# Performance work log

Measured on AMD Instinct MI355X. Metric: run time of the kernel, lower is better.

## Reference

```python
import math
import jax, jax.numpy as jnp
import numpy as np

IN_CH = 64
RANK = 32
W_FREQ = 64


def setup_inputs() -> dict:
    key = jax.random.key(0)
    k1, k2, k3 = jax.random.split(key, 3)
    B, C, H, W = 8, IN_CH, 256, 512
    x = jax.random.normal(k1, (B, C, H, W), dtype=jnp.float32)
    dt = jax.random.uniform(k2, (B,), dtype=jnp.float32)
    # 1x1 conv: weight [out=2*RANK, in=C], bias [2*RANK]; init U(-0.01, 0.01) as in module
    w = jax.random.uniform(k3, (2 * RANK, C), dtype=jnp.float32, minval=-0.01, maxval=0.01)
    b = jnp.zeros((2 * RANK,), dtype=jnp.float32)
    return {"x": x, "dt": dt, "w": w, "b": b}


def reference(x, dt, w, b):
    B, C, H, W = x.shape
    # AdaptiveAvgPool2d((None, W_FREQ)): W divisible by W_FREQ -> exact block mean
    x_pool = x.reshape(B, C, H, W_FREQ, W // W_FREQ).mean(-1)  # [B,C,H,Wf]
    params = jnp.einsum('bchw,oc->bohw', x_pool, w) + b[None, :, None, None]
    nu = jax.nn.softplus(params[:, :RANK])                    # [B,R,H,Wf]
    theta = jnp.tanh(params[:, RANK:]) * math.pi              # [B,R,H,Wf]
    dtb = dt[:, None, None, None]
    decay = jnp.exp(-nu * dtb)
    angle = theta * dtb
    filt_r = (decay * jnp.cos(angle)).sum(axis=1)             # [B,H,Wf]
    filt_i = (decay * jnp.sin(angle)).sum(axis=1)
    filt = (filt_r + 1j * filt_i)[:, None, :, :]              # [B,1,H,Wf] complex64
    x_spec = jnp.fft.rfft2(x, norm='ortho')                   # [B,C,H,W//2+1]
    out_spec = jnp.concatenate([x_spec[..., :W_FREQ] * filt, x_spec[..., W_FREQ:]], axis=-1)
    return jnp.fft.irfft2(out_spec, s=(H, W), norm='ortho').astype(x.dtype)
```

## Files before the change

kernel.cpp:

```cpp
#include <hip/hip_runtime.h>
#include <cstddef>
#include <cstdint>

#define PI_F    3.14159265358979323846f
#define TWOPI_F 6.28318530717958647692f

#define ZH_OFF 16777216u
#define G_OFF  33554432u
#define TW_OFF 33816576u

typedef __attribute__((ext_vector_type(8))) short bf16x8;
typedef __attribute__((ext_vector_type(4))) float f32x4;

__device__ __forceinline__ void bsplit(float x, short& h, short& l) {
    uint32_t u  = __float_as_uint(x);
    uint32_t hb = (u + 0x7fffu + ((u >> 16) & 1u)) & 0xffff0000u;
    h = (short)(hb >> 16);
    float r = x - __uint_as_float(hb);
    uint32_t u2 = __float_as_uint(r);
    l = (short)((u2 + 0x7fffu + ((u2 >> 16) & 1u)) >> 16);
}

__global__ __launch_bounds__(256) void k_filt(const float* __restrict__ x,
                                              const float* __restrict__ dt,
                                              const float* __restrict__ wmat,
                                              const float* __restrict__ bvec,
                                              float* __restrict__ G) {
    __shared__ float pooled[64 * 65];
    __shared__ float wsh[64 * 65];
    int t = threadIdx.x;
    int b = blockIdx.x >> 8, h = blockIdx.x & 255;
    for (int i = t; i < 4096; i += 256)
        wsh[(i >> 6) * 65 + (i & 63)] = wmat[i];
    for (int c = 0; c < 64; c++) {
        const float* xr = x + (((size_t)(b * 64 + c)) * 256 + h) * 512;
        float2 v = ((const float2*)xr)[t];
        float s = v.x + v.y;
        s += __shfl_xor(s, 1);
        s += __shfl_xor(s, 2);
        if ((t & 3) == 0) pooled[c * 65 + (t >> 2)] = s * 0.125f;
    }
    __syncthreads();
    float dtb = dt[b];
    int o = t & 63, q = t >> 6;
    float bo = bvec[o];
    for (int jj = 0; jj < 16; jj++) {
        int j = q * 16 + jj;
        float acc = bo;
        #pragma unroll 16
        for (int c = 0; c < 64; c++)
            acc = fmaf(wsh[o * 65 + c], pooled[c * 65 + j], acc);
        float nl;
        if (o < 32) nl = (acc > 20.0f) ? acc : log1pf(expf(acc));
        else        nl = tanhf(acc) * PI_F;
        float other = __shfl_xor(nl, 32);
        float nu = (o < 32) ? nl : other;
        float th = (o < 32) ? other : nl;
        float decay = expf(-nu * dtb);
        float sa, ca; sincosf(th * dtb, &sa, &ca);
        float tr = decay * ca, ti = decay * sa;
        #pragma unroll
        for (int off = 1; off < 64; off <<= 1) {
            tr += __shfl_xor(tr, off);
            ti += __shfl_xor(ti, off);
        }
        if ((t & 63) == 0) {
            float2 g = make_float2(0.5f * tr - 1.0f, 0.5f * ti);
            ((float2*)G)[((size_t)b * 256 + h) * 64 + j] = g;
        }
    }
}

__global__ __launch_bounds__(256) void k_gemmA(const float* __restrict__ x,
                                               float* __restrict__ Zw) {
    __shared__ __align__(16) float As[32][68];
    __shared__ __align__(16) float Bs[32][64];
    int t = threadIdx.x;
    int row0 = blockIdx.x * 64, n0 = blockIdx.y * 64;
    int lr = t >> 3, lk4 = (t & 7) << 2;
    int bkr = t >> 4, bc4 = (t & 15) << 2;
    int ty = t >> 4, tx = t & 15;
    int wf0 = (n0 + bc4) >> 1;
    float u_r[2], u_i[2], c16r[2], c16i[2], advr[2], advi[2];
    #pragma unroll
    for (int q = 0; q < 2; q++) {
        int wf = wf0 + q;
        float s, c;
        sincosf((float)((bkr * wf) & 511) * (TWOPI_F / 512.0f), &s, &c);
        u_r[q] = c; u_i[q] = -s;
        sincosf((float)((16 * wf) & 511) * (TWOPI_F / 512.0f), &s, &c);
        c16r[q] = c; c16i[q] = -s;
        sincosf((float)((32 * wf) & 511) * (TWOPI_F / 512.0f), &s, &c);
        advr[q] = c; advi[q] = -s;
    }
    float acc[4][4] = {};
    size_t xrow0 = (size_t)(row0 + lr) * 512;
    size_t xrow1 = (size_t)(row0 + lr + 32) * 512;
    for (int k0 = 0; k0 < 512; k0 += 32) {
        __syncthreads();
        {
            float4 v = *(const float4*)(x + xrow0 + k0 + lk4);
            As[lk4 + 0][lr] = v.x; As[lk4 + 1][lr] = v.y;
            As[lk4 + 2][lr] = v.z; As[lk4 + 3][lr] = v.w;
        }
        {
            float4 v = *(const float4*)(x + xrow1 + k0 + lk4);
            int m = lr + 32;
            As[lk4 + 0][m] = v.x; As[lk4 + 1][m] = v.y;
            As[lk4 + 2][m] = v.z; As[lk4 + 3][m] = v.w;
        }
        *(float4*)&Bs[bkr][bc4] = make_float4(u_r[0], u_i[0], u_r[1], u_i[1]);
        {
            float r0 = u_r[0] * c16r[0] - u_i[0] * c16i[0];
            float i0 = u_r[0] * c16i[0] + u_i[0] * c16r[0];
            float r1 = u_r[1] * c16r[1] - u_i[1] * c16i[1];
            float i1 = u_r[1] * c16i[1] + u_i[1] * c16r[1];
            *(float4*)&Bs[bkr + 16][bc4] = make_float4(r0, i0, r1, i1);
        }
        #pragma unroll
        for (int q = 0; q < 2; q++) {
            float nr = u_r[q] * advr[q] - u_i[q] * advi[q];
            float ni = u_r[q] * advi[q] + u_i[q] * advr[q];
            u_r[q] = nr; u_i[q] = ni;
        }
        __syncthreads();
        #pragma unroll
        for (int kk = 0; kk < 32; kk++) {
            float4 ra = *(const float4*)&As[kk][ty << 2];
            float4 rb = *(const float4*)&Bs[kk][tx << 2];
            float a[4] = {ra.x, ra.y, ra.z, ra.w};
            float bq[4] = {rb.x, rb.y, rb.z, rb.w};
            #pragma unroll
            for (int i = 0; i < 4; i++)
                #pragma unroll
                for (int j = 0; j < 4; j++)
                    acc[i][j] = fmaf(a[i], bq[j], acc[i][j]);
        }
    }
    #pragma unroll
    for (int i = 0; i < 4; i++) {
        int r = row0 + (ty << 2) + i;
        *(float4*)(Zw + (size_t)r * 128 + n0 + (tx << 2)) =
            make_float4(acc[i][0], acc[i][1], acc[i][2], acc[i][3]);
    }
}

__global__ __launch_bounds__(256) void k_twid(float* __restrict__ outbase) {
    int t = blockIdx.x * 256 + threadIdx.x;
    int m = t >> 8, k = t & 255;
    float s, c;
    sincosf((float)((m * k) & 255) * (TWOPI_F / 256.0f), &s, &c);
    short ch, cl, nsh, nsl, psh, psl;
    bsplit(c, ch, cl);
    bsplit(-s, nsh, nsl);
    bsplit(s, psh, psl);
    short* fw = (short*)(outbase + TW_OFF);
    short* iv = fw + 262144;
    fw[t] = ch; fw[65536 + t] = cl; fw[131072 + t] = nsh; fw[196608 + t] = nsl;
    iv[t] = ch; iv[65536 + t] = cl; iv[131072 + t] = psh; iv[196608 + t] = psl;
}

__global__ __launch_bounds__(256) void k_cgemm_mfma(const float* __restrict__ Zin,
                                                    float* __restrict__ Zout,
                                                    const float* __restrict__ G,
                                                    const short* __restrict__ tab) {
    __shared__ short As[4][64][40];
    __shared__ short Bs[4][64][40];
    int t = threadIdx.x;
    int p  = blockIdx.x;
    int m0 = blockIdx.y * 64;
    size_t zbase = (size_t)p * 32768;
    int w = t >> 6, l = t & 63;
    int wm = w >> 1, wj = w & 1;
    int lr = l & 15, lh = l >> 4;
    int att = w;
    int bk  = t >> 3;
    int bju = t & 7;

    f32x4 accRp[2][2] = {}, accRm[2][2] = {}, accI[2][2] = {};

    #pragma unroll 1
    for (int k0 = 0; k0 < 256; k0 += 32) {
        __syncthreads();
        {
            const short* tb = tab + att * 65536 + k0;
            #pragma unroll
            for (int i = 0; i < 4; i++) {
                int c = l + 64 * i;
                int row = c >> 2, ko = (c & 3) << 3;
                int4 v = *(const int4*)(tb + (m0 + row) * 256 + ko);
                *(int4*)&As[att][row][ko] = v;
            }
        }
        #pragma unroll
        for (int pass = 0; pass < 4; pass++) {
            int j = 2 * bju + 16 * pass;
            float4 v = *(const float4*)(Zin + zbase + (size_t)(k0 + bk) * 128 + j * 2);
            short h0, l0, h1, l1;
            bsplit(v.x, h0, l0); bsplit(v.y, h1, l1);
            Bs[0][j][bk] = h0; Bs[1][j][bk] = l0; Bs[2][j][bk] = h1; Bs[3][j][bk] = l1;
            bsplit(v.z, h0, l0); bsplit(v.w, h1, l1);
            Bs[0][j + 1][bk] = h0; Bs[1][j + 1][bk] = l0; Bs[2][j + 1][bk] = h1; Bs[3][j + 1][bk] = l1;
        }
        __syncthreads();
        bf16x8 trh[2], trl[2], tih[2], til[2], zrh[2], zrl[2], zih[2], zil[2];
        #pragma unroll
        for (int s = 0; s < 2; s++) {
            int ar = wm * 32 + s * 16 + lr;
            trh[s] = *(const bf16x8*)&As[0][ar][lh << 3];
            trl[s] = *(const bf16x8*)&As[1][ar][lh << 3];
            tih[s] = *(const bf16x8*)&As[2][ar][lh << 3];
            til[s] = *(const bf16x8*)&As[3][ar][lh << 3];
            int br = wj * 32 + s * 16 + lr;
            zrh[s] = *(const bf16x8*)&Bs[0][br][lh << 3];
            zrl[s] = *(const bf16x8*)&Bs[1][br][lh << 3];
            zih[s] = *(const bf16x8*)&Bs[2][br][lh << 3];
            zil[s] = *(const bf16x8*)&Bs[3][br][lh << 3];
        }
        #pragma unroll
        for (int i = 0; i < 2; i++)
            #pragma unroll
            for (int jj = 0; jj < 2; jj++) {
                accRp[i][jj] = __builtin_amdgcn_mfma_f32_16x16x32_bf16(trh[i], zrh[jj], accRp[i][jj], 0, 0, 0);
                accRp[i][jj] = __builtin_amdgcn_mfma_f32_16x16x32_bf16(trh[i], zrl[jj], accRp[i][jj], 0, 0, 0);
                accRp[i][jj] = __builtin_amdgcn_mfma_f32_16x16x32_bf16(trl[i], zrh[jj], accRp[i][jj], 0, 0, 0);
                accRm[i][jj] = __builtin_amdgcn_mfma_f32_16x16x32_bf16(tih[i], zih[jj], accRm[i][jj], 0, 0, 0);
                accRm[i][jj] = __builtin_amdgcn_mfma_f32_16x16x32_bf16(tih[i], zil[jj], accRm[i][jj], 0, 0, 0);
                accRm[i][jj] = __builtin_amdgcn_mfma_f32_16x16x32_bf16(til[i], zih[jj], accRm[i][jj], 0, 0, 0);
                accI[i][jj]  = __builtin_amdgcn_mfma_f32_16x16x32_bf16(trh[i], zih[jj], accI[i][jj], 0, 0, 0);
                accI[i][jj]  = __builtin_amdgcn_mfma_f32_16x16x32_bf16(trh[i], zil[jj], accI[i][jj], 0, 0, 0);
                accI[i][jj]  = __builtin_amdgcn_mfma_f32_16x16x32_bf16(trl[i], zih[jj], accI[i][jj], 0, 0, 0);
                accI[i][jj]  = __builtin_amdgcn_mfma_f32_16x16x32_bf16(tih[i], zrh[jj], accI[i][jj], 0, 0, 0);
                accI[i][jj]  = __builtin_amdgcn_mfma_f32_16x16x32_bf16(tih[i], zrl[jj], accI[i][jj], 0, 0, 0);
                accI[i][jj]  = __builtin_amdgcn_mfma_f32_16x16x32_bf16(til[i], zrh[jj], accI[i][jj], 0, 0, 0);
            }
    }
    int b = p >> 6;
    #pragma unroll
    for (int i = 0; i < 2; i++)
        #pragma unroll
        for (int jj = 0; jj < 2; jj++) {
            int jcol = wj * 32 + jj * 16 + lr;
            #pragma unroll
            for (int r = 0; r < 4; r++) {
                int m = m0 + wm * 32 + i * 16 + (lh << 2) + r;
                float re = accRp[i][jj][r] - accRm[i][jj][r];
                float im = accI[i][jj][r];
                if (G) {
                    float2 g = ((const float2*)G)[((size_t)b * 256 + m) * 64 + jcol];
                    float nr = re * g.x - im * g.y;
                    float ni = re * g.y + im * g.x;
                    re = nr; im = ni;
                }
                ((float2*)(Zout + zbase))[(size_t)m * 64 + jcol] = make_float2(re, im);
            }
        }
}

__global__ __launch_bounds__(256) void k_gemmE(const float* __restrict__ Zc,
                                               const float* __restrict__ x,
                                               float* __restrict__ out,
                                               int rowLo) {
    __shared__ __align__(16) float As[32][68];
    __shared__ __align__(16) float Bs[32][64];
    int t = threadIdx.x;
    int row0 = rowLo + blockIdx.x * 64, n0 = blockIdx.y * 64;
    int lr = t >> 3, lk4 = (t & 7) << 2;
    int bkr = t >> 4, bc4 = (t & 15) << 2;
    int ty = t >> 4, tx = t & 15;
    const float invN = 1.0f / 131072.0f;
    int par = bkr & 1;
    int wfh = bkr >> 1;
    float u_r[4], u_i[4], c8r[4], c8i[4], advr[4], advi[4];
    #pragma unroll
    for (int d = 0; d < 4; d++) {
        int w = n0 + bc4 + d;
        float s, c;
        sincosf((float)((w * wfh) & 511) * (TWOPI_F / 512.0f), &s, &c);
        u_r[d] = c; u_i[d] = -s;
        sincosf((float)((w * 8) & 511) * (TWOPI_F / 512.0f), &s, &c);
        c8r[d] = c; c8i[d] = -s;
        sincosf((float)((w * 16) & 511) * (TWOPI_F / 512.0f), &s, &c);
        advr[d] = c; advi[d] = -s;
    }
    float acc[4][4] = {};
    for (int k0 = 0; k0 < 128; k0 += 32) {
        __syncthreads();
        {
            float4 v = *(const float4*)(Zc + (size_t)(row0 + lr) * 128 + k0 + lk4);
            As[lk4 + 0][lr] = v.x; As[lk4 + 1][lr] = v.y;
            As[lk4 + 2][lr] = v.z; As[lk4 + 3][lr] = v.w;
        }
        {
            float4 v = *(const float4*)(Zc + (size_t)(row0 + lr + 32) * 128 + k0 + lk4);
            int mm = lr + 32;
            As[lk4 + 0][mm] = v.x; As[lk4 + 1][mm] = v.y;
            As[lk4 + 2][mm] = v.z; As[lk4 + 3][mm] = v.w;
        }
        int wf1 = (k0 >> 1) + wfh;
        float a1 = ((wf1 == 0) ? 1.0f : 2.0f) * invN;
        float a2 = 2.0f * invN;
        float b1[4], b2[4];
        #pragma unroll
        for (int d = 0; d < 4; d++) {
            b1[d] = a1 * (par ? u_i[d] : u_r[d]);
            float vr = u_r[d] * c8r[d] - u_i[d] * c8i[d];
            float vi = u_r[d] * c8i[d] + u_i[d] * c8r[d];
            b2[d] = a2 * (par ? vi : vr);
            float nr = u_r[d] * advr[d] - u_i[d] * advi[d];
            float ni = u_r[d] * advi[d] + u_i[d] * advr[d];
            u_r[d] = nr; u_i[d] = ni;
        }
        *(float4*)&Bs[bkr][bc4]      = make_float4(b1[0], b1[1], b1[2], b1[3]);
        *(float4*)&Bs[bkr + 16][bc4] = make_float4(b2[0], b2[1], b2[2], b2[3]);
        __syncthreads();
        #pragma unroll
        for (int kk = 0; kk < 32; kk++) {
            float4 ra = *(const float4*)&As[kk][ty << 2];
            float4 rb = *(const float4*)&Bs[kk][tx << 2];
            float a[4] = {ra.x, ra.y, ra.z, ra.w};
            float bq[4] = {rb.x, rb.y, rb.z, rb.w};
            #pragma unroll
            for (int i = 0; i < 4; i++)
                #pragma unroll
                for (int j = 0; j < 4; j++)
                    acc[i][j] = fmaf(a[i], bq[j], acc[i][j]);
        }
    }
    #pragma unroll
    for (int i = 0; i < 4; i++) {
        int r = row0 + (ty << 2) + i;
        size_t grow = (size_t)r * 512;
        float4 xv = *(const float4*)(x + grow + n0 + (tx << 2));
        *(float4*)(out + grow + n0 + (tx << 2)) =
            make_float4(acc[i][0] + xv.x, acc[i][1] + xv.y,
                        acc[i][2] + xv.z, acc[i][3] + xv.w);
    }
}

__global__ __launch_bounds__(256) void k_copy(const float* __restrict__ src,
                                              float* __restrict__ dst) {
    int i = blockIdx.x * 256 + threadIdx.x;
    ((float4*)dst)[i] = ((const float4*)src)[i];
}

extern "C" void kernel_launch(void* const* d_in, const int* in_sizes, int n_in,
                              void* d_out, int out_size, void* d_ws, size_t ws_size,
                              hipStream_t stream) {
    (void)in_sizes; (void)n_in; (void)out_size; (void)ws_size;
    const float* x    = (const float*)d_in[0];
    const float* dt   = (const float*)d_in[1];
    const float* wmat = (const float*)d_in[2];
    const float* bvec = (const float*)d_in[3];
    float* out = (float*)d_out;
    float* ws  = (float*)d_ws;

    float* G   = out + G_OFF;
    float* Zw  = out;
    float* Zh  = out + ZH_OFF;
    float* Zc  = out;
    float* stg = ws;
    const short* tabF = (const short*)(out + TW_OFF);
    const short* tabI = tabF + 262144;

    k_filt <<<2048,            256, 0, stream>>>(x, dt, wmat, bvec, G);
    k_twid <<<256,             256, 0, stream>>>(out);
    k_gemmA<<<dim3(2048, 2),   256, 0, stream>>>(x, Zw);
    k_cgemm_mfma<<<dim3(512, 4), 256, 0, stream>>>(Zw, Zh, G, tabF);
    k_cgemm_mfma<<<dim3(512, 4), 256, 0, stream>>>(Zh, Zc, nullptr, tabI);
    k_copy <<<64,              256, 0, stream>>>(Zc, stg);
    k_gemmE<<<dim3(1536, 8),   256, 0, stream>>>(Zc,  x, out, 128 * 256);
    k_gemmE<<<dim3(384, 8),    256, 0, stream>>>(Zc,  x, out, 32 * 256);
    k_gemmE<<<dim3(96, 8),     256, 0, stream>>>(Zc,  x, out, 8 * 256);
    k_gemmE<<<dim3(24, 8),     256, 0, stream>>>(Zc,  x, out, 2 * 256);
    k_gemmE<<<dim3(8, 8),      256, 0, stream>>>(stg, x, out, 0);
}
```

Measured before the change: 1.154 ms.

## Replace FP32 row-DFT GEMM with split-bf16 MFMA using precomputed twiddle table

```diff
diff --git a/kernel.cpp b/kernel.cpp
--- a/kernel.cpp
+++ b/kernel.cpp
@@ -5,11 +5,13 @@
 #define PI_F    3.14159265358979323846f
 #define TWOPI_F 6.28318530717958647692f
 
-#define ZH_OFF 16777216u
-#define G_OFF  33554432u
-#define TW_OFF 33816576u
+#define ZH_OFF  16777216u
+#define G_OFF   33554432u
+#define TW_OFF  33816576u
+#define TWA_OFF 34078720u
 
 typedef __attribute__((ext_vector_type(8))) short bf16x8;
+typedef __attribute__((ext_vector_type(4))) short s16x4;
 typedef __attribute__((ext_vector_type(4))) float f32x4;
 
 __device__ __forceinline__ void bsplit(float x, short& h, short& l) {
@@ -71,80 +73,6 @@
     }
 }
 
-__global__ __launch_bounds__(256) void k_gemmA(const float* __restrict__ x,
-                                               float* __restrict__ Zw) {
-    __shared__ __align__(16) float As[32][68];
-    __shared__ __align__(16) float Bs[32][64];
-    int t = threadIdx.x;
-    int row0 = blockIdx.x * 64, n0 = blockIdx.y * 64;
-    int lr = t >> 3, lk4 = (t & 7) << 2;
-    int bkr = t >> 4, bc4 = (t & 15) << 2;
-    int ty = t >> 4, tx = t & 15;
-    int wf0 = (n0 + bc4) >> 1;
-    float u_r[2], u_i[2], c16r[2], c16i[2], advr[2], advi[2];
-    #pragma unroll
-    for (int q = 0; q < 2; q++) {
-        int wf = wf0 + q;
-        float s, c;
-        sincosf((float)((bkr * wf) & 511) * (TWOPI_F / 512.0f), &s, &c);
-        u_r[q] = c; u_i[q] = -s;
-        sincosf((float)((16 * wf) & 511) * (TWOPI_F / 512.0f), &s, &c);
-        c16r[q] = c; c16i[q] = -s;
-        sincosf((float)((32 * wf) & 511) * (TWOPI_F / 512.0f), &s, &c);
-        advr[q] = c; advi[q] = -s;
-    }
-    float acc[4][4] = {};
-    size_t xrow0 = (size_t)(row0 + lr) * 512;
-    size_t xrow1 = (size_t)(row0 + lr + 32) * 512;
-    for (int k0 = 0; k0 < 512; k0 += 32) {
-        __syncthreads();
-        {
-            float4 v = *(const float4*)(x + xrow0 + k0 + lk4);
-            As[lk4 + 0][lr] = v.x; As[lk4 + 1][lr] = v.y;
-            As[lk4 + 2][lr] = v.z; As[lk4 + 3][lr] = v.w;
-        }
-        {
-            float4 v = *(const float4*)(x + xrow1 + k0 + lk4);
-            int m = lr + 32;
-            As[lk4 + 0][m] = v.x; As[lk4 + 1][m] = v.y;
-            As[lk4 + 2][m] = v.z; As[lk4 + 3][m] = v.w;
-        }
-        *(float4*)&Bs[bkr][bc4] = make_float4(u_r[0], u_i[0], u_r[1], u_i[1]);
-        {
-            float r0 = u_r[0] * c16r[0] - u_i[0] * c16i[0];
-            float i0 = u_r[0] * c16i[0] + u_i[0] * c16r[0];
-            float r1 = u_r[1] * c16r[1] - u_i[1] * c16i[1];
-            float i1 = u_r[1] * c16i[1] + u_i[1] * c16r[1];
-            *(float4*)&Bs[bkr + 16][bc4] = make_float4(r0, i0, r1, i1);
-        }
-        #pragma unroll
-        for (int q = 0; q < 2; q++) {
-            float nr = u_r[q] * advr[q] - u_i[q] * advi[q];
-            float ni = u_r[q] * advi[q] + u_i[q] * advr[q];
-            u_r[q] = nr; u_i[q] = ni;
-        }
-        __syncthreads();
-        #pragma unroll
-        for (int kk = 0; kk < 32; kk++) {
-            float4 ra = *(const float4*)&As[kk][ty << 2];
-            float4 rb = *(const float4*)&Bs[kk][tx << 2];
-            float a[4] = {ra.x, ra.y, ra.z, ra.w};
-            float bq[4] = {rb.x, rb.y, rb.z, rb.w};
-            #pragma unroll
-            for (int i = 0; i < 4; i++)
-                #pragma unroll
-                for (int j = 0; j < 4; j++)
-                    acc[i][j] = fmaf(a[i], bq[j], acc[i][j]);
-        }
-    }
-    #pragma unroll
-    for (int i = 0; i < 4; i++) {
-        int r = row0 + (ty << 2) + i;
-        *(float4*)(Zw + (size_t)r * 128 + n0 + (tx << 2)) =
-            make_float4(acc[i][0], acc[i][1], acc[i][2], acc[i][3]);
-    }
-}
-
 __global__ __launch_bounds__(256) void k_twid(float* __restrict__ outbase) {
     int t = blockIdx.x * 256 + threadIdx.x;
     int m = t >> 8, k = t & 255;
@@ -158,6 +86,94 @@
     short* iv = fw + 262144;
     fw[t] = ch; fw[65536 + t] = cl; fw[131072 + t] = nsh; fw[196608 + t] = nsl;
     iv[t] = ch; iv[65536 + t] = cl; iv[131072 + t] = psh; iv[196608 + t] = psl;
+}
+
+__global__ __launch_bounds__(256) void k_twidA(float* __restrict__ outbase) {
+    int t = blockIdx.x * 256 + threadIdx.x;
+    int n = t >> 9, ww = t & 511;
+    int wf = n >> 1;
+    float s, c;
+    sincosf((float)((ww * wf) & 511) * (TWOPI_F / 512.0f), &s, &c);
+    float val = (n & 1) ? -s : c;
+    short h, lo; bsplit(val, h, lo);
+    short* ta = (short*)(outbase + TWA_OFF);
+    ta[t] = h;
+    ta[65536 + t] = lo;
+}
+
+__global__ __launch_bounds__(256) void k_gemmA_mfma(const float* __restrict__ x,
+                                                    float* __restrict__ Zw,
+                                                    const short* __restrict__ tabA) {
+    __shared__ short As[2][64][40];
+    __shared__ short Bs[2][128][40];
+    int t = threadIdx.x;
+    int row0 = blockIdx.x * 64;
+    int w = t >> 6, l = t & 63;
+    int wm = w >> 1, wj = w & 1;
+    int lr = l & 15, lh = l >> 4;
+    f32x4 acc[2][4] = {};
+    #pragma unroll 1
+    for (int k0 = 0; k0 < 512; k0 += 32) {
+        __syncthreads();
+        #pragma unroll
+        for (int rep = 0; rep < 2; rep++) {
+            int f = t + 256 * rep;
+            int r = f >> 3, c4 = (f & 7) << 2;
+            float4 v = *(const float4*)(x + (size_t)(row0 + r) * 512 + k0 + c4);
+            s16x4 hv, lv;
+            short h, lo;
+            bsplit(v.x, h, lo); hv.x = h; lv.x = lo;
+            bsplit(v.y, h, lo); hv.y = h; lv.y = lo;
+            bsplit(v.z, h, lo); hv.z = h; lv.z = lo;
+            bsplit(v.w, h, lo); hv.w = h; lv.w = lo;
+            *(s16x4*)&As[0][r][c4] = hv;
+            *(s16x4*)&As[1][r][c4] = lv;
+        }
+        {
+            int comp = t >> 7, u = t & 127;
+            const short* tb = tabA + comp * 65536 + k0;
+            #pragma unroll
+            for (int q = 0; q < 4; q++) {
+                int f = u * 4 + q;
+                int n = f >> 2, ko = (f & 3) << 3;
+                int4 v = *(const int4*)(tb + n * 512 + ko);
+                *(int4*)&Bs[comp][n][ko] = v;
+            }
+        }
+        __syncthreads();
+        bf16x8 ah[2], al[2], bh[4], bl[4];
+        #pragma unroll
+        for (int s = 0; s < 2; s++) {
+            int ar = wm * 32 + s * 16 + lr;
+            ah[s] = *(const bf16x8*)&As[0][ar][lh << 3];
+            al[s] = *(const bf16x8*)&As[1][ar][lh << 3];
+        }
+        #pragma unroll
+        for (int j = 0; j < 4; j++) {
+            int bn = wj * 64 + j * 16 + lr;
+            bh[j] = *(const bf16x8*)&Bs[0][bn][lh << 3];
+            bl[j] = *(const bf16x8*)&Bs[1][bn][lh << 3];
+        }
+        #pragma unroll
+        for (int s = 0; s < 2; s++)
+            #pragma unroll
+            for (int j = 0; j < 4; j++) {
+                acc[s][j] = __builtin_amdgcn_mfma_f32_16x16x32_bf16(ah[s], bh[j], acc[s][j], 0, 0, 0);
+                acc[s][j] = __builtin_amdgcn_mfma_f32_16x16x32_bf16(ah[s], bl[j], acc[s][j], 0, 0, 0);
+                acc[s][j] = __builtin_amdgcn_mfma_f32_16x16x32_bf16(al[s], bh[j], acc[s][j], 0, 0, 0);
+            }
+    }
+    #pragma unroll
+    for (int s = 0; s < 2; s++)
+        #pragma unroll
+        for (int j = 0; j < 4; j++) {
+            int col = wj * 64 + j * 16 + lr;
+            #pragma unroll
+            for (int r4 = 0; r4 < 4; r4++) {
+                int r = row0 + wm * 32 + s * 16 + (lh << 2) + r4;
+                Zw[(size_t)r * 128 + col] = acc[s][j][r4];
+            }
+        }
 }
 
 __global__ __launch_bounds__(256) void k_cgemm_mfma(const float* __restrict__ Zin,
@@ -362,10 +378,12 @@
     float* stg = ws;
     const short* tabF = (const short*)(out + TW_OFF);
     const short* tabI = tabF + 262144;
+    const short* tabA = (const short*)(out + TWA_OFF);
 
     k_filt <<<2048,            256, 0, stream>>>(x, dt, wmat, bvec, G);
     k_twid <<<256,             256, 0, stream>>>(out);
-    k_gemmA<<<dim3(2048, 2),   256, 0, stream>>>(x, Zw);
+    k_twidA<<<256,             256, 0, stream>>>(out);
+    k_gemmA_mfma<<<2048,       256, 0, stream>>>(x, Zw, tabA);
     k_cgemm_mfma<<<dim3(512, 4), 256, 0, stream>>>(Zw, Zh, G, tabF);
     k_cgemm_mfma<<<dim3(512, 4), 256, 0, stream>>>(Zh, Zc, nullptr, tabI);
     k_copy <<<64,              256, 0, stream>>>(Zc, stg);
```

Measured after the change: 1.013 ms. -12.2%, faster.
